# Performance work log

Measured on AMD Instinct MI355X. Metric: run time of the kernel, lower is better.

## Reference

```python
import jax, jax.numpy as jnp
import numpy as np

G, HQ, D = 8, 4, 64        # kv groups, query heads per group, head size
S, HID = 2048, 2048        # tokens (single prefill sequence), hidden size
SCALE = D ** -0.5


def _rope(x, cos, sin):
    # x: [S, ..., D]; cos/sin: [S, D//2]; GPT-NeoX rotate-half style
    half = D // 2
    shape = (S,) + (1,) * (x.ndim - 2) + (half,)
    c = cos.reshape(shape)
    s = sin.reshape(shape)
    x1, x2 = x[..., :half], x[..., half:]
    return jnp.concatenate([x1 * c - x2 * s, x2 * c + x1 * s], axis=-1)


def setup_inputs() -> dict:
    key = jax.random.key(0)
    k1, k2, k3 = jax.random.split(key, 3)
    hidden_states = jax.random.normal(k1, (S, HID), dtype=jnp.float32)
    w_qkv = jax.random.normal(k2, (HID, G * (HQ + 2) * D), dtype=jnp.float32) * 0.02
    w_dense = jax.random.normal(k3, (HID, HID), dtype=jnp.float32) * 0.02
    inv_freq = 1.0 / (10000.0 ** (jnp.arange(0, D, 2, dtype=jnp.float32) / D))
    freqs = jnp.arange(S, dtype=jnp.float32)[:, None] * inv_freq[None, :]  # [S, D//2]
    return {"hidden_states": hidden_states, "cos": jnp.cos(freqs), "sin": jnp.sin(freqs),
            "w_qkv": w_qkv, "w_dense": w_dense}


def reference(hidden_states, cos, sin, w_qkv, w_dense):
    qkv = hidden_states @ w_qkv                       # [S, G*(HQ+2)*D]
    qkv = qkv.reshape(S, G, HQ + 2, D)
    q = qkv[:, :, :HQ]                                # [S, G, HQ, D]
    k = qkv[:, :, HQ]                                 # [S, G, D]
    v = qkv[:, :, HQ + 1]                             # [S, G, D]
    q = _rope(q, cos, sin)
    k = _rope(k, cos, sin)
    # causal GQA attention (prefill path, single sequence)
    scores = jnp.einsum('sghd,tgd->ghst', q, k) * SCALE   # [G, HQ, S, S]
    causal = jnp.tril(jnp.ones((S, S), dtype=bool))
    scores = jnp.where(causal, scores, jnp.float32(-1e30))
    attn = jax.nn.softmax(scores, axis=-1)
    out = jnp.einsum('ghst,tgd->sghd', attn, v)           # [S, G, HQ, D]
    return out.reshape(S, G * HQ * D) @ w_dense
```

## Files before the change

### kernel.cpp

```cpp
#include <hip/hip_runtime.h>

#define S_LEN 2048
#define HID_DIM 2048
#define NG 8
#define NHQ 4
#define DH 64
#define QSCALE 0.18033688011112042f
#define FIXMAX 12.0f

typedef short short8 __attribute__((ext_vector_type(8)));
typedef float f32x4 __attribute__((ext_vector_type(4)));
typedef unsigned short ushort_t;

__device__ __forceinline__ unsigned short f2bf(float f) {
  unsigned u = __builtin_bit_cast(unsigned, f);
  u += 0x7fffu + ((u >> 16) & 1u);
  return (unsigned short)(u >> 16);
}

__device__ __forceinline__ void mfma16(f32x4& d, short8 a, short8 b) {
  asm volatile("v_mfma_f32_16x16x32_bf16 %0, %1, %2, %0" : "+v"(d) : "v"(a), "v"(b));
}

#define GLDS16(gp, lp) __builtin_amdgcn_global_load_lds( \
    (__attribute__((address_space(1))) void*)(gp),       \
    (__attribute__((address_space(3))) void*)(lp), 16, 0, 0)

__global__ __launch_bounds__(256) void cvt_bf16_k(const float* __restrict__ in,
                                                  ushort_t* __restrict__ out, int n4) {
  int i = blockIdx.x * 256 + threadIdx.x;
  if (i >= n4) return;
  float4 v = ((const float4*)in)[i];
  ushort4 o;
  o.x = f2bf(v.x); o.y = f2bf(v.y); o.z = f2bf(v.z); o.w = f2bf(v.w);
  ((ushort4*)out)[i] = o;
}

__global__ __launch_bounds__(256) void tcvt_k(const float* __restrict__ in,
                                              ushort_t* __restrict__ out, int R, int C) {
  __shared__ ushort_t t[32][33];
  int bx = blockIdx.x * 32, by = blockIdx.y * 32;
  int tx = threadIdx.x & 31, ty = threadIdx.x >> 5;
  for (int j = ty; j < 32; j += 8)
    t[j][tx] = f2bf(in[(long)(by + j) * C + bx + tx]);
  __syncthreads();
  for (int j = ty; j < 32; j += 8)
    out[(long)(bx + j) * R + by + tx] = t[tx][j];
}

__global__ __launch_bounds__(256) void cs_trans_k(const float* __restrict__ cosb,
                                                  const float* __restrict__ sinb,
                                                  float* __restrict__ cosT,
                                                  float* __restrict__ sinT) {
  int idx = blockIdx.x * 256 + threadIdx.x;
  int s = idx >> 5, i = idx & 31;
  cosT[i * 2048 + s] = cosb[s * 32 + i];
  sinT[i * 2048 + s] = sinb[s * 32 + i];
}

#define GEMM_PROLOG64()                                                     \
  const int tid = threadIdx.x;                                              \
  const int w = tid >> 6, lane = tid & 63;                                  \
  const int m0 = blockIdx.y * 128, n0 = blockIdx.x * 64;                    \
  const int sl = lane >> 3;                                                 \
  const int sc = (lane & 7) ^ sl;                                           \
  const ushort_t* Ag = A + (size_t)(m0 + 32 * w + sl) * K + sc * 8;         \
  const ushort_t* Bg = BT + (size_t)(n0 + 16 * w + sl) * K + sc * 8;        \
  f32x4 acc[2][4];                                                          \
  _Pragma("unroll") for (int i = 0; i < 2; ++i)                             \
  _Pragma("unroll") for (int j = 0; j < 4; ++j)                             \
      acc[i][j] = (f32x4){0.f, 0.f, 0.f, 0.f};                              \
  const int fr = lane & 15;                                                 \
  const int kq4 = lane >> 4;

#define GEMM_KLOOP64()                                                     \
  for (int kt = 0; kt < K; kt += 64) {                                     \
    GLDS16(Ag,          &Al[(32 * w) * 64]);                               \
    GLDS16(Ag +  8 * K, &Al[(32 * w + 8) * 64]);                           \
    GLDS16(Ag + 16 * K, &Al[(32 * w + 16) * 64]);                          \
    GLDS16(Ag + 24 * K, &Al[(32 * w + 24) * 64]);                          \
    GLDS16(Bg,          &Bl[(16 * w) * 64]);                               \
    GLDS16(Bg +  8 * K, &Bl[(16 * w + 8) * 64]);                           \
    Ag += 64; Bg += 64;                                                    \
    __syncthreads();                                                       \
    _Pragma("unroll")                                                      \
    for (int c = 0; c < 2; ++c) {                                          \
      short8 af[2], bfr[4];                                                \
      _Pragma("unroll") for (int mf = 0; mf < 2; ++mf) {                   \
        const int row = 32 * w + 16 * mf + fr;                             \
        af[mf] = *(const short8*)&Al[row * 64 +                            \
                 (((kq4 + 4 * c) ^ (row & 7)) << 3)];                      \
      }                                                                    \
      _Pragma("unroll") for (int nf = 0; nf < 4; ++nf) {                   \
        const int row = 16 * nf + fr;                                      \
        bfr[nf] = *(const short8*)&Bl[row * 64 +                           \
                  (((kq4 + 4 * c) ^ (row & 7)) << 3)];                     \
      }                                                                    \
      _Pragma("unroll") for (int mf = 0; mf < 2; ++mf)                     \
      _Pragma("unroll") for (int nf = 0; nf < 4; ++nf)                     \
          mfma16(acc[mf][nf], af[mf], bfr[nf]);                            \
    }                                                                      \
    __syncthreads();                                                       \
  }

__global__ __launch_bounds__(256) void gemm_bt_k(const ushort_t* __restrict__ A,
                                                 const ushort_t* __restrict__ BT,
                                                 float* __restrict__ C,
                                                 int M, int N, int K) {
  __shared__ __align__(16) ushort_t Al[128 * 64];
  __shared__ __align__(16) ushort_t Bl[64 * 64];
  GEMM_PROLOG64();
  GEMM_KLOOP64();
  const int crow = m0 + 32 * w + 4 * (lane >> 4);
  const int ccol = n0 + fr;
#pragma unroll
  for (int mf = 0; mf < 2; ++mf)
#pragma unroll
    for (int nf = 0; nf < 4; ++nf)
#pragma unroll
      for (int r = 0; r < 4; ++r)
        C[(size_t)(crow + 16 * mf + r) * N + ccol + 16 * nf] = acc[mf][nf][r];
}

__global__ __launch_bounds__(256) void gemm_qkv_k(const ushort_t* __restrict__ A,
                                                  const ushort_t* __restrict__ BT,
                                                  const float* __restrict__ cosT,
                                                  const float* __restrict__ sinT,
                                                  ushort_t* __restrict__ Qbf,
                                                  ushort_t* __restrict__ Kbf,
                                                  ushort_t* __restrict__ Vbuf,
                                                  int M, int N, int K) {
  __shared__ __align__(16) ushort_t Al[128 * 64];
  __shared__ __align__(16) ushort_t Bl[64 * 64];
  GEMM_PROLOG64();
  GEMM_KLOOP64();
  const int crow = m0 + 32 * w + 4 * (lane >> 4);
  const int hb = blockIdx.x % 6;
  const int gg = blockIdx.x / 6;
  if (hb == 5) {
    ushort_t* dst = Vbuf + (size_t)gg * 2048 * 64;
#pragma unroll
    for (int mf = 0; mf < 2; ++mf)
#pragma unroll
      for (int nf = 0; nf < 4; ++nf)
#pragma unroll
        for (int r = 0; r < 4; ++r)
          dst[(size_t)(crow + 16 * mf + r) * 64 + 16 * nf + fr] =
              f2bf(acc[mf][nf][r]);
  } else {
    const float qs = (hb < 4) ? QSCALE : 1.0f;
    ushort_t* dst = (hb < 4) ? Qbf + (size_t)(gg * 4 + hb) * 2048 * 64
                             : Kbf + (size_t)gg * 2048 * 64;
#pragma unroll
    for (int mf = 0; mf < 2; ++mf) {
#pragma unroll
      for (int nf2 = 0; nf2 < 2; ++nf2) {
        const int i = 16 * nf2 + fr;
        float4 cT = *(const float4*)&cosT[(size_t)i * 2048 + crow + 16 * mf];
        float4 sT = *(const float4*)&sinT[(size_t)i * 2048 + crow + 16 * mf];
        const float cc[4] = {cT.x, cT.y, cT.z, cT.w};
        const float ss[4] = {sT.x, sT.y, sT.z, sT.w};
#pragma unroll
        for (int r = 0; r < 4; ++r) {
          const size_t row = crow + 16 * mf + r;
          float x1 = acc[mf][nf2][r], x2 = acc[mf][nf2 + 2][r];
          dst[row * 64 + i]      = f2bf((x1 * cc[r] - x2 * ss[r]) * qs);
          dst[row * 64 + i + 32] = f2bf((x2 * cc[r] + x1 * ss[r]) * qs);
        }
      }
    }
  }
}

__global__ __launch_bounds__(256) void vtrans_k(const ushort_t* __restrict__ Vbuf,
                                                ushort_t* __restrict__ Vt) {
  __shared__ ushort_t t[64][65];
  int s0 = blockIdx.x * 64, g = blockIdx.y;
  for (int idx = threadIdx.x; idx < 4096; idx += 256) {
    int r = idx >> 6, d = idx & 63;
    t[d][r] = Vbuf[((size_t)g * 2048 + s0 + r) * 64 + d];
  }
  __syncthreads();
  for (int idx = threadIdx.x; idx < 4096; idx += 256) {
    int d = idx >> 6, c = idx & 63;
    Vt[((size_t)g * 64 + d) * 2048 + s0 + c] = t[d][c];
  }
}

__global__ __launch_bounds__(256, 4) void attn9_k(const ushort_t* __restrict__ Qbf,
                                                  const ushort_t* __restrict__ Kbf,
                                                  const ushort_t* __restrict__ Vt,
                                                  ushort_t* __restrict__ outb) {
  __shared__ __align__(16) ushort_t Kl[2][64 * 64];
  __shared__ __align__(16) ushort_t Vl[2][64 * 64];
  __shared__ __align__(16) ushort_t Pl[4][1024];
  const int gh = blockIdx.x;
  const int y = blockIdx.y;
  const int bb = y & 7, aa = y >> 3;
  const int u = (aa == 0) ? 31 - bb : (aa == 1) ? 16 + bb : (aa == 2) ? 15 - bb : bb;
  const int g = gh >> 2;
  const int w = threadIdx.x >> 6, l = threadIdx.x & 63;
  const int li = l & 15, hi = l >> 4;
  const int q0 = 64 * u + 16 * w;
  const int nt = u + 1;

  const ushort_t* Qh = Qbf + (long)gh * 2048 * 64;
  const ushort_t* Kh = Kbf + (long)g * 2048 * 64;
  const ushort_t* Vh = Vt + (long)g * 64 * 2048;
  char* Pw = (char*)&Pl[w][0];

  const int sr = 16 * w + (l >> 3);
  const int sc = (l & 7) ^ (l >> 3);
  const short8 ones = {0x3F80, 0x3F80, 0x3F80, 0x3F80, 0x3F80, 0x3F80, 0x3F80, 0x3F80};

  short8 aq0 = *(const short8*)&Qh[(q0 + li) * 64 + hi * 8];
  short8 aq1 = *(const short8*)&Qh[(q0 + li) * 64 + 32 + hi * 8];

  f32x4 o[4];
#pragma unroll
  for (int df = 0; df < 4; ++df) o[df] = (f32x4){0.f, 0.f, 0.f, 0.f};
  f32x4 os = (f32x4){0.f, 0.f, 0.f, 0.f};

  GLDS16(Kh + (long)sr * 64 + sc * 8,         &Kl[0][(16 * w) * 64]);
  GLDS16(Kh + (long)(sr + 8) * 64 + sc * 8,   &Kl[0][(16 * w + 8) * 64]);
  GLDS16(Vh + (long)sr * 2048 + sc * 8,       &Vl[0][(16 * w) * 64]);
  GLDS16(Vh + (long)(sr + 8) * 2048 + sc * 8, &Vl[0][(16 * w + 8) * 64]);
  __syncthreads();

  int buf = 0;
  for (int it = 0; it < nt; ++it) {
    const int t0 = it * 64;
    if (it + 1 < nt) {
      const int tn = t0 + 64;
      GLDS16(Kh + (long)(tn + sr) * 64 + sc * 8,       &Kl[buf ^ 1][(16 * w) * 64]);
      GLDS16(Kh + (long)(tn + sr + 8) * 64 + sc * 8,   &Kl[buf ^ 1][(16 * w + 8) * 64]);
      GLDS16(Vh + (long)sr * 2048 + tn + sc * 8,       &Vl[buf ^ 1][(16 * w) * 64]);
      GLDS16(Vh + (long)(sr + 8) * 2048 + tn + sc * 8, &Vl[buf ^ 1][(16 * w + 8) * 64]);
    }
    const ushort_t* kb = &Kl[buf][0];
    const ushort_t* vb = &Vl[buf][0];

    f32x4 sf[4];
#pragma unroll
    for (int f = 0; f < 4; ++f) sf[f] = (f32x4){0.f, 0.f, 0.f, 0.f};
    __builtin_amdgcn_s_setprio(1);
#pragma unroll
    for (int f = 0; f < 4; ++f) {
      const int row = 16 * f + li;
      short8 b0 = *(const short8*)&kb[row * 64 + ((hi ^ (row & 7)) << 3)];
      short8 b1 = *(const short8*)&kb[row * 64 + (((hi + 4) ^ (row & 7)) << 3)];
      mfma16(sf[f], aq0, b0);
      mfma16(sf[f], aq1, b1);
    }
    __builtin_amdgcn_s_setprio(0);

    if (t0 + 63 > q0) {
#pragma unroll
      for (int f = 0; f < 4; ++f) {
        int t = t0 + 16 * f + li;
#pragma unroll
        for (int r = 0; r < 4; ++r)
          if (t > q0 + 4 * hi + r) sf[f][r] = -1e30f;
      }
    }
#pragma unroll
    for (int f = 0; f < 4; ++f) {
      int k2 = 2 * (li + 16 * f);
#pragma unroll
      for (int r = 0; r < 4; ++r) {
        float p = __builtin_amdgcn_exp2f(sf[f][r] - FIXMAX);
        int q = 4 * hi + r;
        *(ushort_t*)(Pw + q * 128 + (k2 ^ ((q & 7) << 4))) =
            (ushort_t)(__builtin_bit_cast(unsigned, p) >> 16);
      }
    }

    __builtin_amdgcn_s_setprio(1);
#pragma unroll
    for (int kst = 0; kst < 2; ++kst) {
      short8 pa = *(const short8*)(Pw + li * 128 + (((4 * kst + hi) ^ (li & 7)) << 4));
#pragma unroll
      for (int df = 0; df < 4; ++df) {
        const int row = 16 * df + li;
        short8 bv = *(const short8*)&vb[row * 64 + (((4 * kst + hi) ^ (row & 7)) << 3)];
        mfma16(o[df], pa, bv);
      }
      mfma16(os, pa, ones);
    }
    __builtin_amdgcn_s_setprio(0);

    __syncthreads();
    buf ^= 1;
  }
#pragma unroll
  for (int r = 0; r < 4; ++r) {
    float inv = 1.f / os[r];
#pragma unroll
    for (int df = 0; df < 4; ++df)
      outb[(long)(q0 + 4 * hi + r) * HID_DIM + gh * 64 + 16 * df + li] =
          f2bf(o[df][r] * inv);
  }
}

extern "C" void kernel_launch(void* const* d_in, const int* in_sizes, int n_in,
                              void* d_out, int out_size, void* d_ws, size_t ws_size,
                              hipStream_t stream) {
  const float* X    = (const float*)d_in[0];
  const float* cosb = (const float*)d_in[1];
  const float* sinb = (const float*)d_in[2];
  const float* Wqkv = (const float*)d_in[3];
  const float* Wd   = (const float*)d_in[4];
  float* out = (float*)d_out;

  char* ws = (char*)d_ws;
  ushort_t* Xbf   = (ushort_t*)ws;
  ushort_t* WqkvT = Xbf + (size_t)2048 * 2048;
  ushort_t* WdT   = WqkvT + (size_t)3072 * 2048;
  ushort_t* Qbf   = WdT + (size_t)2048 * 2048;
  ushort_t* Kbf   = Qbf + (size_t)32 * 2048 * 64;
  ushort_t* Vbuf  = Kbf + (size_t)8 * 2048 * 64;
  ushort_t* Vt    = Vbuf + (size_t)8 * 2048 * 64;
  ushort_t* attnO = Vt + (size_t)8 * 2048 * 64;
  float*    cosT  = (float*)(attnO + (size_t)2048 * 2048);
  float*    sinT  = cosT + (size_t)32 * 2048;

  cvt_bf16_k<<<4096, 256, 0, stream>>>(X, Xbf, (2048 * 2048) / 4);
  tcvt_k<<<dim3(3072 / 32, 2048 / 32), 256, 0, stream>>>(Wqkv, WqkvT, 2048, 3072);
  tcvt_k<<<dim3(2048 / 32, 2048 / 32), 256, 0, stream>>>(Wd, WdT, 2048, 2048);
  cs_trans_k<<<256, 256, 0, stream>>>(cosb, sinb, cosT, sinT);

  gemm_qkv_k<<<dim3(3072 / 64, 2048 / 128), 256, 0, stream>>>(
      Xbf, WqkvT, cosT, sinT, Qbf, Kbf, Vbuf, 2048, 3072, 2048);

  vtrans_k<<<dim3(S_LEN / 64, NG), 256, 0, stream>>>(Vbuf, Vt);

  attn9_k<<<dim3(NG * NHQ, 32), 256, 0, stream>>>(Qbf, Kbf, Vt, attnO);

  gemm_bt_k<<<dim3(2048 / 64, 2048 / 128), 256, 0, stream>>>(attnO, WdT, out,
                                                             2048, 2048, 2048);
}
```

Baseline: 138.5 us.

## Merge prep kernels into one launch and write V transposed from QKV GEMM

```diff
diff --git a/kernel.cpp b/kernel.cpp
--- a/kernel.cpp
+++ b/kernel.cpp
@@ -26,36 +26,49 @@
     (__attribute__((address_space(1))) void*)(gp),       \
     (__attribute__((address_space(3))) void*)(lp), 16, 0, 0)
 
-__global__ __launch_bounds__(256) void cvt_bf16_k(const float* __restrict__ in,
-                                                  ushort_t* __restrict__ out, int n4) {
-  int i = blockIdx.x * 256 + threadIdx.x;
-  if (i >= n4) return;
-  float4 v = ((const float4*)in)[i];
-  ushort4 o;
-  o.x = f2bf(v.x); o.y = f2bf(v.y); o.z = f2bf(v.z); o.w = f2bf(v.w);
-  ((ushort4*)out)[i] = o;
-}
-
-__global__ __launch_bounds__(256) void tcvt_k(const float* __restrict__ in,
-                                              ushort_t* __restrict__ out, int R, int C) {
+__global__ __launch_bounds__(256) void prep_k(const float* __restrict__ X,
+                                              const float* __restrict__ Wqkv,
+                                              const float* __restrict__ Wd,
+                                              const float* __restrict__ cosb,
+                                              const float* __restrict__ sinb,
+                                              ushort_t* __restrict__ Xbf,
+                                              ushort_t* __restrict__ WqkvT,
+                                              ushort_t* __restrict__ WdT,
+                                              float* __restrict__ cosT,
+                                              float* __restrict__ sinT) {
   __shared__ ushort_t t[32][33];
-  int bx = blockIdx.x * 32, by = blockIdx.y * 32;
-  int tx = threadIdx.x & 31, ty = threadIdx.x >> 5;
-  for (int j = ty; j < 32; j += 8)
-    t[j][tx] = f2bf(in[(long)(by + j) * C + bx + tx]);
-  __syncthreads();
-  for (int j = ty; j < 32; j += 8)
-    out[(long)(bx + j) * R + by + tx] = t[tx][j];
-}
-
-__global__ __launch_bounds__(256) void cs_trans_k(const float* __restrict__ cosb,
-                                                  const float* __restrict__ sinb,
-                                                  float* __restrict__ cosT,
-                                                  float* __restrict__ sinT) {
-  int idx = blockIdx.x * 256 + threadIdx.x;
-  int s = idx >> 5, i = idx & 31;
-  cosT[i * 2048 + s] = cosb[s * 32 + i];
-  sinT[i * 2048 + s] = sinb[s * 32 + i];
+  const int b = blockIdx.x;
+  if (b < 4096) {
+    int i = b * 256 + threadIdx.x;
+    float4 v = ((const float4*)X)[i];
+    ushort4 o;
+    o.x = f2bf(v.x); o.y = f2bf(v.y); o.z = f2bf(v.z); o.w = f2bf(v.w);
+    ((ushort4*)Xbf)[i] = o;
+  } else if (b < 14336) {
+    const float* in;
+    ushort_t* out;
+    int R, C, bx, by;
+    if (b < 10240) {
+      int idx = b - 4096;
+      in = Wqkv; out = WqkvT; R = 2048; C = 3072;
+      bx = (idx % 96) * 32; by = (idx / 96) * 32;
+    } else {
+      int idx = b - 10240;
+      in = Wd; out = WdT; R = 2048; C = 2048;
+      bx = (idx % 64) * 32; by = (idx / 64) * 32;
+    }
+    int tx = threadIdx.x & 31, ty = threadIdx.x >> 5;
+    for (int j = ty; j < 32; j += 8)
+      t[j][tx] = f2bf(in[(size_t)(by + j) * C + bx + tx]);
+    __syncthreads();
+    for (int j = ty; j < 32; j += 8)
+      out[(size_t)(bx + j) * R + by + tx] = t[tx][j];
+  } else {
+    int idx = (b - 14336) * 256 + threadIdx.x;
+    int s = idx >> 5, i = idx & 31;
+    cosT[i * 2048 + s] = cosb[s * 32 + i];
+    sinT[i * 2048 + s] = sinb[s * 32 + i];
+  }
 }
 
 #define GEMM_PROLOG64()                                                     \
@@ -128,7 +141,7 @@
                                                   const float* __restrict__ sinT,
                                                   ushort_t* __restrict__ Qbf,
                                                   ushort_t* __restrict__ Kbf,
-                                                  ushort_t* __restrict__ Vbuf,
+                                                  ushort_t* __restrict__ Vt,
                                                   int M, int N, int K) {
   __shared__ __align__(16) ushort_t Al[128 * 64];
   __shared__ __align__(16) ushort_t Bl[64 * 64];
@@ -138,15 +151,18 @@
   const int hb = blockIdx.x % 6;
   const int gg = blockIdx.x / 6;
   if (hb == 5) {
-    ushort_t* dst = Vbuf + (size_t)gg * 2048 * 64;
+    ushort_t* dst = Vt + (size_t)gg * 64 * 2048;
 #pragma unroll
     for (int mf = 0; mf < 2; ++mf)
 #pragma unroll
-      for (int nf = 0; nf < 4; ++nf)
-#pragma unroll
-        for (int r = 0; r < 4; ++r)
-          dst[(size_t)(crow + 16 * mf + r) * 64 + 16 * nf + fr] =
-              f2bf(acc[mf][nf][r]);
+      for (int nf = 0; nf < 4; ++nf) {
+        ushort4 o;
+        o.x = f2bf(acc[mf][nf][0]);
+        o.y = f2bf(acc[mf][nf][1]);
+        o.z = f2bf(acc[mf][nf][2]);
+        o.w = f2bf(acc[mf][nf][3]);
+        *(ushort4*)&dst[(size_t)(16 * nf + fr) * 2048 + crow + 16 * mf] = o;
+      }
   } else {
     const float qs = (hb < 4) ? QSCALE : 1.0f;
     ushort_t* dst = (hb < 4) ? Qbf + (size_t)(gg * 4 + hb) * 2048 * 64
@@ -169,21 +185,6 @@
         }
       }
     }
-  }
-}
-
-__global__ __launch_bounds__(256) void vtrans_k(const ushort_t* __restrict__ Vbuf,
-                                                ushort_t* __restrict__ Vt) {
-  __shared__ ushort_t t[64][65];
-  int s0 = blockIdx.x * 64, g = blockIdx.y;
-  for (int idx = threadIdx.x; idx < 4096; idx += 256) {
-    int r = idx >> 6, d = idx & 63;
-    t[d][r] = Vbuf[((size_t)g * 2048 + s0 + r) * 64 + d];
-  }
-  __syncthreads();
-  for (int idx = threadIdx.x; idx < 4096; idx += 256) {
-    int d = idx >> 6, c = idx & 63;
-    Vt[((size_t)g * 64 + d) * 2048 + s0 + c] = t[d][c];
   }
 }
 
@@ -318,21 +319,16 @@
   ushort_t* WdT   = WqkvT + (size_t)3072 * 2048;
   ushort_t* Qbf   = WdT + (size_t)2048 * 2048;
   ushort_t* Kbf   = Qbf + (size_t)32 * 2048 * 64;
-  ushort_t* Vbuf  = Kbf + (size_t)8 * 2048 * 64;
-  ushort_t* Vt    = Vbuf + (size_t)8 * 2048 * 64;
+  ushort_t* Vt    = Kbf + (size_t)8 * 2048 * 64;
   ushort_t* attnO = Vt + (size_t)8 * 2048 * 64;
   float*    cosT  = (float*)(attnO + (size_t)2048 * 2048);
   float*    sinT  = cosT + (size_t)32 * 2048;
 
-  cvt_bf16_k<<<4096, 256, 0, stream>>>(X, Xbf, (2048 * 2048) / 4);
-  tcvt_k<<<dim3(3072 / 32, 2048 / 32), 256, 0, stream>>>(Wqkv, WqkvT, 2048, 3072);
-  tcvt_k<<<dim3(2048 / 32, 2048 / 32), 256, 0, stream>>>(Wd, WdT, 2048, 2048);
-  cs_trans_k<<<256, 256, 0, stream>>>(cosb, sinb, cosT, sinT);
+  prep_k<<<14592, 256, 0, stream>>>(X, Wqkv, Wd, cosb, sinb,
+                                    Xbf, WqkvT, WdT, cosT, sinT);
 
   gemm_qkv_k<<<dim3(3072 / 64, 2048 / 128), 256, 0, stream>>>(
-      Xbf, WqkvT, cosT, sinT, Qbf, Kbf, Vbuf, 2048, 3072, 2048);
-
-  vtrans_k<<<dim3(S_LEN / 64, NG), 256, 0, stream>>>(Vbuf, Vt);
+      Xbf, WqkvT, cosT, sinT, Qbf, Kbf, Vt, 2048, 3072, 2048);
 
   attn9_k<<<dim3(NG * NHQ, 32), 256, 0, stream>>>(Qbf, Kbf, Vt, attnO);
 
```

Measured after the change: 127.8 us. 1.08x faster.
